# Kernel tuning notes

Hardware: AMD Instinct MI355X
Metric: run time of the kernel (lower is better)

## Reference

```python
import jax, jax.numpy as jnp
import numpy as np

EPS = 0.1       # TopK_custom default epsilon (SOFT top-k)
MAX_ITER = 50   # max_iter=50 in source
K = 400         # tks1/tks2/tks3 k


def soft_topk(scores, k, epsilon=EPS, max_iter=MAX_ITER):
    """SOFT differentiable top-k via Sinkhorn (Xie et al.), anchors {0,1}.
    scores: [bs, n] (finite; the -inf masking branch of the original is a no-op
    here since inputs are post-ReLU activations). Returns soft top-k mask [bs, n].
    """
    bs, n = scores.shape
    anchors = jnp.asarray([0.0, 1.0], dtype=scores.dtype).reshape(1, 1, 2)
    C = (scores[:, :, None] - anchors) ** 2            # [bs, n, 2]
    C = C / jax.lax.stop_gradient(jnp.max(C))
    mu = jnp.ones((1, n, 1), scores.dtype) / n
    nu = jnp.asarray([k / n, (n - k) / n], dtype=scores.dtype).reshape(1, 1, 2)
    G = jnp.exp(-C / epsilon)                          # [bs, n, 2]

    def step(carry, _):
        _, v = carry
        u = mu / jnp.sum(G * v, axis=-1, keepdims=True)   # [bs, n, 1]
        v = nu / jnp.sum(G * u, axis=-2, keepdims=True)   # [bs, 1, 2]
        return (u, v), None

    u0 = jnp.ones((bs, n, 1), scores.dtype)
    v0 = jnp.ones((bs, 1, 2), scores.dtype) / 2.0
    (u, v), _ = jax.lax.scan(step, (u0, v0), None, length=max_iter)
    gamma0 = (u * G * v)[:, :, 0]                      # transport mass to anchor 1... column 0
    return gamma0 * n


def setup_inputs() -> dict:
    key = jax.random.key(0)
    ks = jax.random.split(key, 6)
    bs, d_in, d_h, d_out = 4096, 1024, 500, 10
    sc = lambda f: 1.0 / np.sqrt(f)
    return {
        "x":  jax.random.normal(ks[0], (bs, d_in), jnp.float32),
        "W1": jax.random.normal(ks[1], (d_in, d_h), jnp.float32) * sc(d_in),
        "b1": jnp.zeros((d_h,), jnp.float32),
        "W2": jax.random.normal(ks[2], (d_h, d_h), jnp.float32) * sc(d_h),
        "b2": jnp.zeros((d_h,), jnp.float32),
        "W3": jax.random.normal(ks[3], (d_h, d_h), jnp.float32) * sc(d_h),
        "b3": jnp.zeros((d_h,), jnp.float32),
        "W4": jax.random.normal(ks[4], (d_h, d_out), jnp.float32) * sc(d_h),
        "b4": jnp.zeros((d_out,), jnp.float32),
        "sparse": 1,
    }


def reference(x, W1, b1, W2, b2, W3, b3, W4, b4, sparse):
    s = jnp.asarray(sparse, x.dtype)
    out = jax.nn.relu(x @ W1 + b1)
    out = out * s * soft_topk(out, K) + (1.0 - s) * out
    out = jax.nn.relu(out @ W2 + b2)
    out = out * s * soft_topk(out, K) + (1.0 - s) * out
    out = jax.nn.relu(out @ W3 + b3)
    out = out * s * soft_topk(out, K) + (1.0 - s) * out
    return out @ W4 + b4
```

## Files before the change

kernel.cpp:

```cpp
#include <hip/hip_runtime.h>
#include <math.h>


typedef __attribute__((ext_vector_type(8))) short short8;
typedef __attribute__((ext_vector_type(8))) _Float16 half8;
typedef __attribute__((ext_vector_type(4))) float f32x4;

__device__ __forceinline__ short f2h(float v) {
  _Float16 h = (_Float16)v;
  return *(short*)&h;
}
__device__ __forceinline__ float h2f(short s) {
  _Float16 h = *(_Float16*)&s;
  return (float)h;
}

template <int CTRL>
__device__ __forceinline__ float dpp_mov0(float v) {
  return __int_as_float(__builtin_amdgcn_update_dpp(
      0, __float_as_int(v), CTRL, 0xf, 0xf, true));
}
__device__ __forceinline__ float wave_sum(float v) {
  v += dpp_mov0<0x111>(v);
  v += dpp_mov0<0x112>(v);
  v += dpp_mov0<0x114>(v);
  v += dpp_mov0<0x118>(v);
  v += dpp_mov0<0x142>(v);
  v += dpp_mov0<0x143>(v);
  return __int_as_float(__builtin_amdgcn_readlane(__float_as_int(v), 63));
}
__device__ __forceinline__ float wave_max_nn(float v) {
  v = fmaxf(v, dpp_mov0<0x111>(v));
  v = fmaxf(v, dpp_mov0<0x112>(v));
  v = fmaxf(v, dpp_mov0<0x114>(v));
  v = fmaxf(v, dpp_mov0<0x118>(v));
  v = fmaxf(v, dpp_mov0<0x142>(v));
  v = fmaxf(v, dpp_mov0<0x143>(v));
  return __int_as_float(__builtin_amdgcn_readlane(__float_as_int(v), 63));
}

struct MegaArgs {
  const float *x, *W1, *b1, *W2, *b2, *W3, *b3, *W4, *b4;
  const int* sparse;
  float* out;
  short *Ablk, *B1blk, *B2blk, *B3blk, *Hmblk;
  float *H, *bp, *cmaxA;
};

__device__ __forceinline__ void store8h(short* dst, const float* v) {
  short hi[8];
  #pragma unroll
  for (int i = 0; i < 8; ++i) hi[i] = f2h(v[i]);
  *(uint4*)dst = *(const uint4*)hi;
}
__device__ __forceinline__ void store16h(short* dstHi, short* dstLo,
                                         const float* v) {
  short hi[8], lo[8];
  #pragma unroll
  for (int i = 0; i < 8; ++i) {
    hi[i] = f2h(v[i]);
    lo[i] = f2h(v[i] - h2f(hi[i]));
  }
  *(uint4*)dstHi = *(const uint4*)hi;
  *(uint4*)dstLo = *(const uint4*)lo;
}

#define LDF(t, va, vb)                                                   \
  do {                                                                   \
    const int ta_ = ((t) < NTK) ? (t) : (t) - NTK;                       \
    const short* Ag_ = Abase + (size_t)ta_ * 2048;                       \
    const short* Bg_ = Bbase + (size_t)(t) * 2048;                       \
    va[0] = *(const short8*)(Ag_);                                       \
    va[1] = *(const short8*)(Ag_ + 512);                                 \
    va[2] = *(const short8*)(Ag_ + 1024);                                \
    va[3] = *(const short8*)(Ag_ + 1536);                                \
    vb[0] = *(const short8*)(Bg_);                                       \
    vb[1] = *(const short8*)(Bg_ + 512);                                 \
    vb[2] = *(const short8*)(Bg_ + 1024);                                \
    vb[3] = *(const short8*)(Bg_ + 1536);                                \
  } while (0)

#define CMP(va, vb)                                                      \
  do {                                                                   \
    _Pragma("unroll")                                                    \
    for (int s_ = 0; s_ < 4; ++s_)                                       \
      _Pragma("unroll")                                                  \
      for (int u_ = 0; u_ < 4; ++u_)                                     \
        acc[s_][u_] = __builtin_amdgcn_mfma_f32_16x16x32_f16(            \
            *(const half8*)&va[s_], *(const half8*)&vb[u_],              \
            acc[s_][u_], 0, 0, 0);                                       \
  } while (0)

template <int NTK>
__global__ __launch_bounds__(256, 2) void gemm_k(
    const short* __restrict__ Ablk, const short* __restrict__ Bblk,
    const float* __restrict__ bp, float* __restrict__ H,
    float* __restrict__ cmaxArr)
{
  __shared__ __align__(16) float fl[8704];
  __shared__ float red4[4];

  const int tid  = threadIdx.x;
  const int lane = tid & 63, w = tid >> 6;
  const int rg = lane >> 4, rl = lane & 15;

  const int by = blockIdx.x & 63, bx = blockIdx.x >> 6;
  const int row0 = by * 64, col0 = bx * 64;

  const short* Abase = Ablk + (size_t)by * NTK * 2048 + lane * 8;
  const short* Bbase = Bblk + (size_t)bx * (2 * NTK) * 2048 + lane * 8;

  constexpr int nt = (2 * NTK) >> 2;
  const int t0 = w * nt;

  f32x4 acc[4][4];
  #pragma unroll
  for (int s = 0; s < 4; ++s)
    #pragma unroll
    for (int u = 0; u < 4; ++u)
      acc[s][u] = (f32x4){0.f, 0.f, 0.f, 0.f};

  short8 A0[4], B0[4], A1[4], B1[4], A2[4], B2[4], A3[4], B3[4];
  LDF(t0 + 0, A0, B0);
  LDF(t0 + 1, A1, B1);
  LDF(t0 + 2, A2, B2);
  LDF(t0 + 3, A3, B3);
  #pragma unroll
  for (int i = 0; i < nt; i += 4) {
    CMP(A0, B0);
    if (i + 4 < nt) LDF(t0 + i + 4, A0, B0);
    CMP(A1, B1);
    if (i + 5 < nt) LDF(t0 + i + 5, A1, B1);
    CMP(A2, B2);
    if (i + 6 < nt) LDF(t0 + i + 6, A2, B2);
    CMP(A3, B3);
    if (i + 7 < nt) LDF(t0 + i + 7, A3, B3);
  }

  float lmax = 0.0f;
  #pragma unroll
  for (int p = 0; p < 2; ++p) {
    if (p == 1) __syncthreads();
    #pragma unroll
    for (int sp = 0; sp < 2; ++sp) {
      const int s = p * 2 + sp;
      #pragma unroll
      for (int u = 0; u < 4; ++u)
        #pragma unroll
        for (int i = 0; i < 4; ++i)
          fl[w * 2176 + (sp * 16 + rg * 4 + i) * 68 + u * 16 + rl] = acc[s][u][i];
    }
    __syncthreads();

    const int rloc = w * 8 + (lane >> 3);
    const int c0 = (lane & 7) * 8;
    f32x4 s0 = {0.f, 0.f, 0.f, 0.f}, s1 = {0.f, 0.f, 0.f, 0.f};
    #pragma unroll
    for (int q = 0; q < 4; ++q) {
      const float* src = fl + q * 2176 + rloc * 68 + c0;
      s0 += *(const f32x4*)src;
      s1 += *(const f32x4*)(src + 4);
    }
    const int gr = row0 + p * 32 + rloc;
    const int gc = col0 + c0;
    const f32x4 bb0 = *(const f32x4*)&bp[gc];
    const f32x4 bb1 = *(const f32x4*)&bp[gc + 4];
    f32x4 o0, o1;
    #pragma unroll
    for (int i = 0; i < 4; ++i) {
      o0[i] = fmaxf(s0[i] + bb0[i], 0.f);
      o1[i] = fmaxf(s1[i] + bb1[i], 0.f);
    }
    float* Hp = H + (size_t)gr * 512 + gc;
    *(f32x4*)Hp = o0;
    *(f32x4*)(Hp + 4) = o1;
    #pragma unroll
    for (int i = 0; i < 4; ++i) {
      if (gc + i < 500) {
        const float v = o0[i], vm = v - 1.0f;
        lmax = fmaxf(lmax, fmaxf(v * v, vm * vm));
      }
      if (gc + 4 + i < 500) {
        const float v = o1[i], vm = v - 1.0f;
        lmax = fmaxf(lmax, fmaxf(v * v, vm * vm));
      }
    }
  }

  lmax = wave_max_nn(lmax);
  if (lane == 0) red4[w] = lmax;
  __syncthreads();
  if (tid == 0)
    cmaxArr[blockIdx.x] =
        fmaxf(fmaxf(red4[0], red4[1]), fmaxf(red4[2], red4[3]));
}

__global__ __launch_bounds__(256) void prep_k(MegaArgs a)
{
  const int sIdx = threadIdx.x;
  const int m = ((sIdx >> 6) << 4) | (sIdx & 15);
  const int g = (sIdx >> 4) & 3;
  for (int job = blockIdx.x; job < 2561; job += gridDim.x) {
    if (job < 2048) {
      const int p = job >> 5, t = job & 31;
      const float* src = a.x + (size_t)(p * 64 + m) * 1024 + t * 32 + g * 8;
      float v[8];
      const f32x4 u0 = *(const f32x4*)src;
      const f32x4 u1 = *(const f32x4*)(src + 4);
      #pragma unroll
      for (int i = 0; i < 4; ++i) { v[i] = u0[i]; v[4 + i] = u1[i]; }
      short* d = a.Ablk + ((size_t)p * 32 + t) * 2048 + sIdx * 8;
      store8h(d, v);
    } else if (job < 2304) {
      const int j = job - 2048;
      const int p = j >> 5, t = j & 31;
      const int n = p * 64 + m;
      float v[8];
      #pragma unroll
      for (int i = 0; i < 8; ++i) {
        const int k = t * 32 + g * 8 + i;
        v[i] = (n < 500) ? a.W1[(size_t)k * 500 + n] : 0.0f;
      }
      short* d = a.B1blk + ((size_t)p * 64 + t) * 2048 + sIdx * 8;
      store16h(d, d + 65536, v);
    } else if (job < 2560) {
      const int j = (job - 2304) & 127;
      const bool isW3 = (job >= 2432);
      const float* W = isW3 ? a.W3 : a.W2;
      short* Bb = isW3 ? a.B3blk : a.B2blk;
      const int p = j >> 4, t = j & 15;
      const int n = p * 64 + m;
      float v[8];
      #pragma unroll
      for (int i = 0; i < 8; ++i) {
        const int k = t * 32 + g * 8 + i;
        v[i] = (n < 500 && k < 500) ? W[(size_t)k * 500 + n] : 0.0f;
      }
      short* d = Bb + ((size_t)p * 32 + t) * 2048 + sIdx * 8;
      store16h(d, d + 32768, v);
    } else {
      for (int r = 0; r < 6; ++r) {
        const int idx = r * 256 + threadIdx.x;
        const int L = idx >> 9, c = idx & 511;
        const float* src = (L == 0) ? a.b1 : (L == 1) ? a.b2 : a.b3;
        a.bp[idx] = (c < 500) ? src[c] : 0.0f;
      }
    }
  }
}

__device__ __forceinline__ void softk_row(
    const float* __restrict__ H, const float* __restrict__ cmaxArr,
    float s, int row, int lane, float* mh)
{
  const f32x4 cc0 = *(const f32x4*)&cmaxArr[lane * 8];
  const f32x4 cc1 = *(const f32x4*)&cmaxArr[lane * 8 + 4];
  float cmax = fmaxf(fmaxf(fmaxf(cc0[0], cc0[1]), fmaxf(cc0[2], cc0[3])),
                     fmaxf(fmaxf(cc1[0], cc1[1]), fmaxf(cc1[2], cc1[3])));
  cmax = wave_max_nn(cmax);

  const float inv = 1.0f / (0.1f * cmax);
  const float* Hr = H + (size_t)row * 512 + lane * 8;
  const f32x4 u0 = *(const f32x4*)Hr;
  const f32x4 u1 = *(const f32x4*)(Hr + 4);
  float h[8] = {u0[0], u0[1], u0[2], u0[3], u1[0], u1[1], u1[2], u1[3]};
  float R[8];
  #pragma unroll
  for (int j = 0; j < 8; ++j) R[j] = __expf((2.0f * h[j] - 1.0f) * inv);

  const int nval = min(max(500 - lane * 8, 0), 8);

  float u_lo = -40.0f, u_hi = 40.0f;
  float uu = 0.0f, t = 1.0f, A = 0.0f;
  for (int it = 0; it < 50; ++it) {
    float Ap = 0.0f, Sp = 0.0f;
    #pragma unroll
    for (int j = 0; j < 8; ++j) {
      float wv = __builtin_amdgcn_rcpf(fmaf(t, R[j], 1.0f));
      if (j >= nval) wv = 0.0f;
      Ap += wv;
      Sp = fmaf(wv, wv, Sp);
    }
    A = wave_sum(Ap);
    const float S = wave_sum(Sp);
    if (fabsf(A - 400.0f) < 0.01f || it == 49) break;
    if (A > 400.0f) u_lo = uu; else u_hi = uu;
    const float du = (A - 400.0f) * __builtin_amdgcn_rcpf(A - S);
    float un = uu + du;
    if (!(un > u_lo && un < u_hi)) un = 0.5f * (u_lo + u_hi);
    uu = un;
    t = __expf(uu);
  }

  const float kA = 400.0f / A;
  #pragma unroll
  for (int j = 0; j < 8; ++j) {
    const float wv = __builtin_amdgcn_rcpf(fmaf(t, R[j], 1.0f));
    float o = h[j] * (s * (kA * wv) + (1.0f - s));
    if (j >= nval) o = 0.0f;
    mh[j] = o;
  }
}

__global__ __launch_bounds__(512) void sinkhorn_mid(
    MegaArgs a, const float* __restrict__ cmaxArr, short* __restrict__ outBlk)
{
  __shared__ float lf[8 * 64 * 9];
  const int w    = threadIdx.x >> 6;
  const int lane = threadIdx.x & 63;
  const int r0   = blockIdx.x * 8;
  const int row  = r0 + w;

  float mh[8];
  softk_row(a.H, cmaxArr, (float)a.sparse[0], row, lane, mh);

  #pragma unroll
  for (int j = 0; j < 8; ++j)
    lf[j * 576 + lane * 9 + w] = mh[j];
  __syncthreads();

  const int p     = r0 >> 6;
  const int q     = (r0 & 63) >> 4;
  const int base8 = r0 & 8;
  const int half = lane >> 5, lh = lane & 31;
  const int tt = 2 * w + half;
  const int g = (lh >> 3) & 3, rr = lh & 7;

  float v[8];
  #pragma unroll
  for (int j = 0; j < 8; ++j)
    v[j] = lf[j * 576 + (tt * 4 + g) * 9 + rr];

  const int slot = q * 64 + g * 16 + base8 + rr;
  short* o = outBlk + ((size_t)p * 16 + tt) * 2048 + slot * 8;
  store8h(o, v);
}

__global__ __launch_bounds__(256) void sinkhorn_fin(
    MegaArgs a, const float* __restrict__ cmaxArr)
{
  const int w    = threadIdx.x >> 6;
  const int lane = threadIdx.x & 63;
  const int row  = blockIdx.x * 4 + w;

  float mh[8];
  softk_row(a.H, cmaxArr, (float)a.sparse[0], row, lane, mh);

  const int nval = min(max(500 - lane * 8, 0), 8);
  float acc[10];
  #pragma unroll
  for (int o = 0; o < 10; ++o) acc[o] = 0.0f;
  const float* Wr = a.W4 + (size_t)lane * 80;
  #pragma unroll
  for (int j = 0; j < 8; ++j) {
    if (j < nval) {
      #pragma unroll
      for (int o = 0; o < 10; ++o)
        acc[o] = fmaf(mh[j], Wr[j * 10 + o], acc[o]);
    }
  }
  #pragma unroll
  for (int o = 0; o < 10; ++o) acc[o] = wave_sum(acc[o]);
  if (lane == 0) {
    #pragma unroll
    for (int o = 0; o < 10; ++o)
      a.out[(size_t)row * 10 + o] = acc[o] + a.b4[o];
  }
}

extern "C" void kernel_launch(void* const* d_in, const int* in_sizes, int n_in,
                              void* d_out, int out_size, void* d_ws, size_t ws_size,
                              hipStream_t stream)
{
  char* ws = (char*)d_ws;

  MegaArgs a;
  a.x  = (const float*)d_in[0];
  a.W1 = (const float*)d_in[1];
  a.b1 = (const float*)d_in[2];
  a.W2 = (const float*)d_in[3];
  a.b2 = (const float*)d_in[4];
  a.W3 = (const float*)d_in[5];
  a.b3 = (const float*)d_in[6];
  a.W4 = (const float*)d_in[7];
  a.b4 = (const float*)d_in[8];
  a.sparse = (const int*)d_in[9];
  a.out = (float*)d_out;

  a.cmaxA = (float*)ws;
  a.bp    = (float*)(ws + 8192);
  a.Ablk  = (short*)(ws + 16384);
  a.B1blk = a.Ablk  + (size_t)64 * 32 * 2048;
  a.B2blk = a.B1blk + (size_t)8 * 64 * 2048;
  a.B3blk = a.B2blk + (size_t)8 * 32 * 2048;
  a.H     = (float*)(a.B3blk + (size_t)8 * 32 * 2048);
  a.Hmblk = (short*)(a.H + (size_t)4096 * 512);

  prep_k<<<512, 256, 0, stream>>>(a);
  gemm_k<32><<<512, 256, 0, stream>>>(a.Ablk, a.B1blk, a.bp, a.H, a.cmaxA);
  sinkhorn_mid<<<512, 512, 0, stream>>>(a, a.cmaxA, a.Hmblk);
  gemm_k<16><<<512, 256, 0, stream>>>(a.Hmblk, a.B2blk, a.bp + 512, a.H,
                                      a.cmaxA + 512);
  sinkhorn_mid<<<512, 512, 0, stream>>>(a, a.cmaxA + 512, a.Hmblk);
  gemm_k<16><<<512, 256, 0, stream>>>(a.Hmblk, a.B3blk, a.bp + 1024, a.H,
                                      a.cmaxA + 1024);
  sinkhorn_fin<<<1024, 256, 0, stream>>>(a, a.cmaxA + 1024);
}
```

Measured before the change: 73.75 us.

## Drop split-fp16 weight compensation and store hidden activations as fp16

Weights were previously split into fp16 hi and lo parts, and the GEMM ran over twice the K tiles to compensate. Now weights are stored as plain fp16, which halves the MFMA work and the B-matrix loads in every GEMM. The intermediate activation buffer H also becomes fp16 instead of fp32, halving its write and read traffic between the GEMM and Sinkhorn kernels. The cost is lower accuracy in the matmuls and in the scores that feed the soft top-k exponentials, which may matter for tolerance.

```diff
diff --git a/kernel.cpp b/kernel.cpp
--- a/kernel.cpp
+++ b/kernel.cpp
@@ -44,7 +44,8 @@
   const int* sparse;
   float* out;
   short *Ablk, *B1blk, *B2blk, *B3blk, *Hmblk;
-  float *H, *bp, *cmaxA;
+  short *H;
+  float *bp, *cmaxA;
 };
 
 __device__ __forceinline__ void store8h(short* dst, const float* v) {
@@ -53,22 +54,10 @@
   for (int i = 0; i < 8; ++i) hi[i] = f2h(v[i]);
   *(uint4*)dst = *(const uint4*)hi;
 }
-__device__ __forceinline__ void store16h(short* dstHi, short* dstLo,
-                                         const float* v) {
-  short hi[8], lo[8];
-  #pragma unroll
-  for (int i = 0; i < 8; ++i) {
-    hi[i] = f2h(v[i]);
-    lo[i] = f2h(v[i] - h2f(hi[i]));
-  }
-  *(uint4*)dstHi = *(const uint4*)hi;
-  *(uint4*)dstLo = *(const uint4*)lo;
-}
 
 #define LDF(t, va, vb)                                                   \
   do {                                                                   \
-    const int ta_ = ((t) < NTK) ? (t) : (t) - NTK;                       \
-    const short* Ag_ = Abase + (size_t)ta_ * 2048;                       \
+    const short* Ag_ = Abase + (size_t)(t) * 2048;                       \
     const short* Bg_ = Bbase + (size_t)(t) * 2048;                       \
     va[0] = *(const short8*)(Ag_);                                       \
     va[1] = *(const short8*)(Ag_ + 512);                                 \
@@ -94,7 +83,7 @@
 template <int NTK>
 __global__ __launch_bounds__(256, 2) void gemm_k(
     const short* __restrict__ Ablk, const short* __restrict__ Bblk,
-    const float* __restrict__ bp, float* __restrict__ H,
+    const float* __restrict__ bp, short* __restrict__ H,
     float* __restrict__ cmaxArr)
 {
   __shared__ __align__(16) float fl[8704];
@@ -108,9 +97,9 @@
   const int row0 = by * 64, col0 = bx * 64;
 
   const short* Abase = Ablk + (size_t)by * NTK * 2048 + lane * 8;
-  const short* Bbase = Bblk + (size_t)bx * (2 * NTK) * 2048 + lane * 8;
-
-  constexpr int nt = (2 * NTK) >> 2;
+  const short* Bbase = Bblk + (size_t)bx * NTK * 2048 + lane * 8;
+
+  constexpr int nt = NTK >> 2;
   const int t0 = w * nt;
 
   f32x4 acc[4][4];
@@ -165,23 +154,17 @@
     const int gc = col0 + c0;
     const f32x4 bb0 = *(const f32x4*)&bp[gc];
     const f32x4 bb1 = *(const f32x4*)&bp[gc + 4];
-    f32x4 o0, o1;
+    float o[8];
     #pragma unroll
     for (int i = 0; i < 4; ++i) {
-      o0[i] = fmaxf(s0[i] + bb0[i], 0.f);
-      o1[i] = fmaxf(s1[i] + bb1[i], 0.f);
-    }
-    float* Hp = H + (size_t)gr * 512 + gc;
-    *(f32x4*)Hp = o0;
-    *(f32x4*)(Hp + 4) = o1;
-    #pragma unroll
-    for (int i = 0; i < 4; ++i) {
+      o[i]     = fmaxf(s0[i] + bb0[i], 0.f);
+      o[4 + i] = fmaxf(s1[i] + bb1[i], 0.f);
+    }
+    store8h(H + (size_t)gr * 512 + gc, o);
+    #pragma unroll
+    for (int i = 0; i < 8; ++i) {
       if (gc + i < 500) {
-        const float v = o0[i], vm = v - 1.0f;
-        lmax = fmaxf(lmax, fmaxf(v * v, vm * vm));
-      }
-      if (gc + 4 + i < 500) {
-        const float v = o1[i], vm = v - 1.0f;
+        const float v = o[i], vm = v - 1.0f;
         lmax = fmaxf(lmax, fmaxf(v * v, vm * vm));
       }
     }
@@ -221,8 +204,8 @@
         const int k = t * 32 + g * 8 + i;
         v[i] = (n < 500) ? a.W1[(size_t)k * 500 + n] : 0.0f;
       }
-      short* d = a.B1blk + ((size_t)p * 64 + t) * 2048 + sIdx * 8;
-      store16h(d, d + 65536, v);
+      short* d = a.B1blk + ((size_t)p * 32 + t) * 2048 + sIdx * 8;
+      store8h(d, v);
     } else if (job < 2560) {
       const int j = (job - 2304) & 127;
       const bool isW3 = (job >= 2432);
@@ -236,8 +219,8 @@
         const int k = t * 32 + g * 8 + i;
         v[i] = (n < 500 && k < 500) ? W[(size_t)k * 500 + n] : 0.0f;
       }
-      short* d = Bb + ((size_t)p * 32 + t) * 2048 + sIdx * 8;
-      store16h(d, d + 32768, v);
+      short* d = Bb + ((size_t)p * 16 + t) * 2048 + sIdx * 8;
+      store8h(d, v);
     } else {
       for (int r = 0; r < 6; ++r) {
         const int idx = r * 256 + threadIdx.x;
@@ -250,7 +233,7 @@
 }
 
 __device__ __forceinline__ void softk_row(
-    const float* __restrict__ H, const float* __restrict__ cmaxArr,
+    const short* __restrict__ H, const float* __restrict__ cmaxArr,
     float s, int row, int lane, float* mh)
 {
   const f32x4 cc0 = *(const f32x4*)&cmaxArr[lane * 8];
@@ -260,11 +243,12 @@
   cmax = wave_max_nn(cmax);
 
   const float inv = 1.0f / (0.1f * cmax);
-  const float* Hr = H + (size_t)row * 512 + lane * 8;
-  const f32x4 u0 = *(const f32x4*)Hr;
-  const f32x4 u1 = *(const f32x4*)(Hr + 4);
-  float h[8] = {u0[0], u0[1], u0[2], u0[3], u1[0], u1[1], u1[2], u1[3]};
-  float R[8];
+  const short* Hr = H + (size_t)row * 512 + lane * 8;
+  const uint4 raw = *(const uint4*)Hr;
+  const short* hs = (const short*)&raw;
+  float h[8], R[8];
+  #pragma unroll
+  for (int j = 0; j < 8; ++j) h[j] = h2f(hs[j]);
   #pragma unroll
   for (int j = 0; j < 8; ++j) R[j] = __expf((2.0f * h[j] - 1.0f) * inv);
 
@@ -391,10 +375,10 @@
   a.bp    = (float*)(ws + 8192);
   a.Ablk  = (short*)(ws + 16384);
   a.B1blk = a.Ablk  + (size_t)64 * 32 * 2048;
-  a.B2blk = a.B1blk + (size_t)8 * 64 * 2048;
-  a.B3blk = a.B2blk + (size_t)8 * 32 * 2048;
-  a.H     = (float*)(a.B3blk + (size_t)8 * 32 * 2048);
-  a.Hmblk = (short*)(a.H + (size_t)4096 * 512);
+  a.B2blk = a.B1blk + (size_t)8 * 32 * 2048;
+  a.B3blk = a.B2blk + (size_t)8 * 16 * 2048;
+  a.H     = a.B3blk + (size_t)8 * 16 * 2048;
+  a.Hmblk = a.H + (size_t)4096 * 512;
 
   prep_k<<<512, 256, 0, stream>>>(a);
   gemm_k<32><<<512, 256, 0, stream>>>(a.Ablk, a.B1blk, a.bp, a.H, a.cmaxA);
```

New measurement: 61.51 us. 16.6% less time.
